# Performance work log

Measured on AMD Instinct MI355X. Metric: run time of the kernel, lower is better.

## Reference

```python
import jax, jax.numpy as jnp
import numpy as np

N = 100000
E = 1600000
F_IN = 128
DIM = 32
NUM_CLASSES = 40
BN_EPS = 1e-5


def setup_inputs() -> dict:
    key = jax.random.key(0)
    ks = jax.random.split(key, 16)
    inp = {}
    inp['x'] = jax.random.normal(ks[0], (N, F_IN), dtype=jnp.float32)
    inp['edge_index'] = jax.random.randint(ks[1], (2, E), 0, N, dtype=jnp.int64)
    s = lambda fan_in: 1.0 / np.sqrt(fan_in)
    # GINConv 1 MLP: Linear(F_IN, DIM) -> ReLU -> Linear(DIM, DIM)
    inp['w1a'] = jax.random.uniform(ks[2], (F_IN, DIM), jnp.float32, -s(F_IN), s(F_IN))
    inp['b1a'] = jnp.zeros((DIM,), jnp.float32)
    inp['w1b'] = jax.random.uniform(ks[3], (DIM, DIM), jnp.float32, -s(DIM), s(DIM))
    inp['b1b'] = jnp.zeros((DIM,), jnp.float32)
    # GINConv 2 MLP: Linear(DIM, DIM) -> ReLU -> Linear(DIM, DIM)
    inp['w2a'] = jax.random.uniform(ks[4], (DIM, DIM), jnp.float32, -s(DIM), s(DIM))
    inp['b2a'] = jnp.zeros((DIM,), jnp.float32)
    inp['w2b'] = jax.random.uniform(ks[5], (DIM, DIM), jnp.float32, -s(DIM), s(DIM))
    inp['b2b'] = jnp.zeros((DIM,), jnp.float32)
    # BatchNorm params (eval mode: running stats)
    inp['bn1_g'] = jnp.ones((DIM,), jnp.float32)
    inp['bn1_b'] = jnp.zeros((DIM,), jnp.float32)
    inp['bn1_m'] = jax.random.normal(ks[6], (DIM,), jnp.float32) * 0.1
    inp['bn1_v'] = jax.random.uniform(ks[7], (DIM,), jnp.float32, 0.5, 1.5)
    inp['bn2_g'] = jnp.ones((DIM,), jnp.float32)
    inp['bn2_b'] = jnp.zeros((DIM,), jnp.float32)
    inp['bn2_m'] = jax.random.normal(ks[8], (DIM,), jnp.float32) * 0.1
    inp['bn2_v'] = jax.random.uniform(ks[9], (DIM,), jnp.float32, 0.5, 1.5)
    # FC heads
    inp['fc1_w'] = jax.random.uniform(ks[10], (DIM, DIM), jnp.float32, -s(DIM), s(DIM))
    inp['fc1_b'] = jnp.zeros((DIM,), jnp.float32)
    inp['fc2_w'] = jax.random.uniform(ks[11], (DIM, NUM_CLASSES), jnp.float32, -s(DIM), s(DIM))
    inp['fc2_b'] = jnp.zeros((NUM_CLASSES,), jnp.float32)
    return inp


def _gin_conv(x, src, dst, wa, ba, wb, bb):
    # sum-aggregate neighbor features (messages flow src -> dst), eps = 0
    agg = jax.ops.segment_sum(x[src], dst, num_segments=N)
    h = agg + x  # (1 + eps) * x + sum_j x_j
    h = jax.nn.relu(h @ wa + ba)
    return h @ wb + bb


def _bn(x, g, b, m, v):
    return (x - m) * (g * jax.lax.rsqrt(v + BN_EPS)) + b


def reference(x, edge_index, w1a, b1a, w1b, b1b, w2a, b2a, w2b, b2b,
              bn1_g, bn1_b, bn1_m, bn1_v, bn2_g, bn2_b, bn2_m, bn2_v,
              fc1_w, fc1_b, fc2_w, fc2_b):
    src, dst = edge_index[0], edge_index[1]
    h = jax.nn.relu(_gin_conv(x, src, dst, w1a, b1a, w1b, b1b))
    h = _bn(h, bn1_g, bn1_b, bn1_m, bn1_v)  # dropout is identity in eval
    h = _gin_conv(h, src, dst, w2a, b2a, w2b, b2b)
    h = _bn(h, bn2_g, bn2_b, bn2_m, bn2_v)
    h = jax.nn.relu(h @ fc1_w + fc1_b)
    logits = h @ fc2_w + fc2_b
    return jax.nn.log_softmax(logits, axis=1)
```

## Files before the change

### kernel.cpp

```cpp
#include <hip/hip_runtime.h>
#include <hip/hip_bf16.h>

static constexpr int N_   = 100000;
static constexpr int E_   = 1600000;
static constexpr int FIN_ = 128;
static constexpr int DIM_ = 32;
static constexpr int NC_  = 40;
static constexpr int NB_BKT = (N_ + 127) / 128;
static constexpr int NCHUNK = 256;
static constexpr int EPC    = E_ / NCHUNK;
static constexpr int PROJ_NB = N_ / 32;
static constexpr int CS_NB  = (NB_BKT + 7) / 8;

__device__ __forceinline__ int edge_at(const void* e, int is64, long long i) {
    return is64 ? (int)((const long long*)e)[i] : ((const int*)e)[i];
}

__device__ __forceinline__ float bflo(unsigned u) { return __uint_as_float(u << 16); }
__device__ __forceinline__ float bfhi(unsigned u) { return __uint_as_float(u & 0xffff0000u); }

#define DETECT_FLAG(edge, sflag)                                        \
    if (threadIdx.x < 64) {                                             \
        const long long* p_ = (const long long*)(edge);                 \
        long long v_ = p_[threadIdx.x];                                 \
        bool bad_ = (v_ < 0 || v_ >= (long long)N_);                    \
        unsigned long long m_ = __ballot(bad_);                         \
        if (threadIdx.x == 0) sflag = (m_ == 0ull) ? 1 : 0;             \
    }                                                                   \
    __syncthreads();

__global__ __launch_bounds__(256) void chist_kernel(const void* __restrict__ edge,
                                                    int* __restrict__ ghist) {
    __shared__ int lh[NB_BKT];
    __shared__ int sflag;
    DETECT_FLAG(edge, sflag)
    for (int i = threadIdx.x; i < NB_BKT; i += 256) lh[i] = 0;
    __syncthreads();
    int f = sflag;
    int b = blockIdx.x;
    int end = b * EPC + EPC;
    for (int e = b * EPC + threadIdx.x; e < end; e += 256) {
        int d = edge_at(edge, f, (long long)E_ + e);
        atomicAdd(&lh[d >> 7], 1);
    }
    __syncthreads();
    for (int i = threadIdx.x; i < NB_BKT; i += 256) ghist[b * NB_BKT + i] = lh[i];
}

__global__ __launch_bounds__(256) void colscan_kernel(const int* __restrict__ ghist,
                                                      int* __restrict__ gcur,
                                                      int* __restrict__ bcnt,
                                                      int* __restrict__ bbase,
                                                      int* __restrict__ offs,
                                                      int* __restrict__ done) {
    __shared__ int tile[256 * 9];
    __shared__ int a[256];
    __shared__ int lastFlag;
    int tid = threadIdx.x;
    int k0 = blockIdx.x * 8;

    {
        int kk = tid & 7, r0 = tid >> 3;
        for (int p = 0; p < 8; ++p) {
            int b = r0 + p * 32;
            int k = k0 + kk;
            tile[b * 9 + kk] = (k < NB_BKT) ? ghist[b * NB_BKT + k] : 0;
        }
    }
    __syncthreads();

    int c = tid >> 5, lane = tid & 31;
    int v[8]; int s = 0;
#pragma unroll
    for (int r = 0; r < 8; ++r) { v[r] = tile[(lane * 8 + r) * 9 + c]; s += v[r]; }
    int incl = s;
#pragma unroll
    for (int off = 1; off < 32; off <<= 1) {
        int u = __shfl_up(incl, off, 32);
        if (lane >= off) incl += u;
    }
    int ex = incl - s;
    int k = k0 + c;
    if (k < NB_BKT) {
        int run = ex;
#pragma unroll
        for (int r = 0; r < 8; ++r) {
            int b = lane * 8 + r;
            gcur[b * NB_BKT + k] = run;
            run += v[r];
        }
        if (lane == 31) bcnt[k] = run;
    }
    __syncthreads();
    if (tid == 0) {
        __threadfence();
        int old = atomicAdd(done, 1);
        lastFlag = (old == CS_NB - 1) ? 1 : 0;
    }
    __syncthreads();
    if (lastFlag) {
        __threadfence();
        int b4[4]; int base4 = tid * 4; int t = 0;
#pragma unroll
        for (int j = 0; j < 4; ++j) { int i = base4 + j; b4[j] = (i < NB_BKT) ? bcnt[i] : 0; t += b4[j]; }
        a[tid] = t;
        __syncthreads();
        for (int off = 1; off < 256; off <<= 1) {
            int u = a[tid] + ((tid >= off) ? a[tid - off] : 0);
            __syncthreads(); a[tid] = u; __syncthreads();
        }
        int g = a[tid] - t;
#pragma unroll
        for (int j = 0; j < 4; ++j) { int i = base4 + j; if (i < NB_BKT) bbase[i] = g; g += b4[j]; }
        if (tid == 255) offs[N_] = a[255];
    }
}

__global__ __launch_bounds__(256) void dscatter_kernel(const void* __restrict__ edge,
                                                       const int* __restrict__ bbase,
                                                       const int* __restrict__ gcur,
                                                       int* __restrict__ packed) {
    __shared__ int cur[NB_BKT];
    __shared__ int sflag;
    DETECT_FLAG(edge, sflag)
    int b = blockIdx.x, tid = threadIdx.x;
    for (int k = tid; k < NB_BKT; k += 256) cur[k] = bbase[k] + gcur[b * NB_BKT + k];
    __syncthreads();
    int f = sflag;
    int end = b * EPC + EPC;
    for (int e = b * EPC + tid; e < end; e += 256) {
        int s = edge_at(edge, f, e);
        int d = edge_at(edge, f, (long long)E_ + e);
        int pos = atomicAdd(&cur[d >> 7], 1);
        packed[pos] = s | ((d & 127) << 17);
    }
}

__global__ __launch_bounds__(256) void fat_kernel(const int* __restrict__ bcnt,
                                                  const int* __restrict__ bbase,
                                                  const int* __restrict__ packed,
                                                  int* __restrict__ offs,
                                                  int* __restrict__ csr,
                                                  const float* __restrict__ x,
                                                  const float* __restrict__ w,
                                                  __hip_bfloat16* __restrict__ yh) {
    __shared__ __align__(16) char smem[32768];
    int tid = threadIdx.x;
    if (blockIdx.x < NB_BKT) {
        int* c   = (int*)smem;
        int* cur = (int*)smem + 128;
        int b = blockIdx.x;
        int beg = bbase[b], cnt = bcnt[b];
        if (tid < 128) c[tid] = 0;
        __syncthreads();
        for (int i = tid; i < cnt; i += 256)
            atomicAdd(&c[packed[beg + i] >> 17], 1);
        __syncthreads();
        int myv = (tid < 128) ? c[tid] : 0;
        for (int off = 1; off < 128; off <<= 1) {
            int t = 0;
            if (tid < 128) t = c[tid] + ((tid >= off) ? c[tid - off] : 0);
            __syncthreads();
            if (tid < 128) c[tid] = t;
            __syncthreads();
        }
        if (tid < 128) {
            int ex = c[tid] - myv;
            cur[tid] = ex;
            int node = b * 128 + tid;
            if (node < N_) offs[node] = beg + ex;
        }
        __syncthreads();
        for (int i = tid; i < cnt; i += 256) {
            int v = packed[beg + i];
            int p = atomicAdd(&cur[v >> 17], 1);
            csr[beg + p] = v & 0x1FFFF;
        }
    } else {
        float* wsm = (float*)smem;
        float* xs  = (float*)(smem + 16384);
        const float4* w4 = (const float4*)w;
        float4* ws4 = (float4*)wsm;
        for (int i = tid; i < FIN_ * DIM_ / 4; i += 256) ws4[i] = w4[i];

        int nodeBase = (blockIdx.x - NB_BKT) * 32;
        const float4* x4 = (const float4*)(x + (size_t)nodeBase * FIN_);
        float4* xs4 = (float4*)xs;
        for (int i = tid; i < 32 * FIN_ / 4; i += 256) xs4[i] = x4[i];
        __syncthreads();

        int d = tid & 31, ns = tid >> 5;
        for (int rep = 0; rep < 4; ++rep) {
            int node = ns + rep * 8;
            float acc = 0.f;
#pragma unroll 4
            for (int k = 0; k < FIN_; ++k) acc += xs[node * FIN_ + k] * wsm[k * DIM_ + d];
            yh[(size_t)(nodeBase + node) * DIM_ + d] = __float2bfloat16(acc);
        }
    }
}

__device__ __forceinline__ void gather_row(const int* __restrict__ csr,
                                           const char* __restrict__ vb,
                                           int beg, int end, int loff,
                                           float& a0, float& a1, float& a2, float& a3) {
    int i = beg;
    for (; i + 3 < end; i += 4) {
        int s0 = csr[i], s1 = csr[i + 1], s2 = csr[i + 2], s3 = csr[i + 3];
        uint2 u0 = *(const uint2*)(vb + (((size_t)s0) << 6) + loff);
        uint2 u1 = *(const uint2*)(vb + (((size_t)s1) << 6) + loff);
        uint2 u2 = *(const uint2*)(vb + (((size_t)s2) << 6) + loff);
        uint2 u3 = *(const uint2*)(vb + (((size_t)s3) << 6) + loff);
        a0 += (bflo(u0.x) + bflo(u1.x)) + (bflo(u2.x) + bflo(u3.x));
        a1 += (bfhi(u0.x) + bfhi(u1.x)) + (bfhi(u2.x) + bfhi(u3.x));
        a2 += (bflo(u0.y) + bflo(u1.y)) + (bflo(u2.y) + bflo(u3.y));
        a3 += (bfhi(u0.y) + bfhi(u1.y)) + (bfhi(u2.y) + bfhi(u3.y));
    }
    for (; i < end; ++i) {
        int s0 = csr[i];
        uint2 u0 = *(const uint2*)(vb + (((size_t)s0) << 6) + loff);
        a0 += bflo(u0.x); a1 += bfhi(u0.x); a2 += bflo(u0.y); a3 += bfhi(u0.y);
    }
}

__global__ __launch_bounds__(256) void aggmlp1_kernel(const int* __restrict__ offs,
                                                      const int* __restrict__ csr,
                                                      const __hip_bfloat16* __restrict__ yh,
                                                      const float* __restrict__ b1a,
                                                      const float* __restrict__ w1b,
                                                      const float* __restrict__ b1b,
                                                      const float* __restrict__ g1,
                                                      const float* __restrict__ be1,
                                                      const float* __restrict__ m1,
                                                      const float* __restrict__ v1,
                                                      const float* __restrict__ w2a,
                                                      __hip_bfloat16* __restrict__ zh) {
    __shared__ float A[32 * 33];
    __shared__ float B[32 * 33];
    __shared__ float w1s[DIM_ * DIM_];
    __shared__ float w2s[DIM_ * DIM_];
    int tid = threadIdx.x;
    for (int i = tid; i < DIM_ * DIM_; i += 256) { w1s[i] = w1b[i]; w2s[i] = w2a[i]; }

    int nl = tid >> 3, lane = tid & 7;
    int node = blockIdx.x * 32 + nl;
    int beg = offs[node], end = offs[node + 1];
    float a0 = 0.f, a1 = 0.f, a2 = 0.f, a3 = 0.f;
    gather_row(csr, (const char*)yh, beg, end, lane << 3, a0, a1, a2, a3);
    {
        float* p = &A[nl * 33 + lane * 4];
        p[0] = a0; p[1] = a1; p[2] = a2; p[3] = a3;
    }
    __syncthreads();

    int d = tid & 31, ng = tid >> 5;
    size_t gbase = (size_t)blockIdx.x * 32 * DIM_;

#pragma unroll
    for (int r = 0; r < 4; ++r) {
        int n = r * 8 + ng;
        float yv = __bfloat162float(yh[gbase + n * DIM_ + d]);
        A[n * 33 + d] = fmaxf(A[n * 33 + d] + yv + b1a[d], 0.f);
    }
    __syncthreads();

    float sc1 = g1[d] * rsqrtf(v1[d] + 1e-5f);
    float sh1 = be1[d] - m1[d] * sc1;

#pragma unroll
    for (int r = 0; r < 4; ++r) {
        int n = r * 8 + ng;
        float s = b1b[d];
#pragma unroll
        for (int k = 0; k < DIM_; ++k) s += A[n * 33 + k] * w1s[k * DIM_ + d];
        B[n * 33 + d] = fmaxf(s, 0.f) * sc1 + sh1;
    }
    __syncthreads();

#pragma unroll
    for (int r = 0; r < 4; ++r) {
        int n = r * 8 + ng;
        float s = 0.f;
#pragma unroll
        for (int k = 0; k < DIM_; ++k) s += B[n * 33 + k] * w2s[k * DIM_ + d];
        zh[gbase + n * DIM_ + d] = __float2bfloat16(s);
    }
}

__global__ __launch_bounds__(256) void aggmlp2_kernel(const int* __restrict__ offs,
                                                      const int* __restrict__ csr,
                                                      const __hip_bfloat16* __restrict__ zh,
                                                      const float* __restrict__ b2a,
                                                      const float* __restrict__ w2b,
                                                      const float* __restrict__ b2b,
                                                      const float* __restrict__ g2,
                                                      const float* __restrict__ be2,
                                                      const float* __restrict__ m2,
                                                      const float* __restrict__ v2,
                                                      const float* __restrict__ f1w,
                                                      const float* __restrict__ f1b,
                                                      const float* __restrict__ f2w,
                                                      const float* __restrict__ f2b,
                                                      float* __restrict__ out) {
    __shared__ float A[32 * 33];
    __shared__ float BC[DIM_ * NC_];
    __shared__ float wA[DIM_ * DIM_];
    __shared__ float wB[DIM_ * DIM_];
    int tid = threadIdx.x;
    for (int i = tid; i < DIM_ * DIM_; i += 256) { wA[i] = w2b[i]; wB[i] = f1w[i]; }

    int nl = tid >> 3, lane = tid & 7;
    int node = blockIdx.x * 32 + nl;
    int beg = offs[node], end = offs[node + 1];
    float a0 = 0.f, a1 = 0.f, a2 = 0.f, a3 = 0.f;
    gather_row(csr, (const char*)zh, beg, end, lane << 3, a0, a1, a2, a3);
    {
        float* p = &A[nl * 33 + lane * 4];
        p[0] = a0; p[1] = a1; p[2] = a2; p[3] = a3;
    }
    __syncthreads();

    int d = tid & 31, ng = tid >> 5;
    size_t gbase = (size_t)blockIdx.x * 32 * DIM_;

#pragma unroll
    for (int r = 0; r < 4; ++r) {
        int n = r * 8 + ng;
        float zv = __bfloat162float(zh[gbase + n * DIM_ + d]);
        A[n * 33 + d] = fmaxf(A[n * 33 + d] + zv + b2a[d], 0.f);
    }
    __syncthreads();

    float sc2 = g2[d] * rsqrtf(v2[d] + 1e-5f);
    float sh2 = be2[d] - m2[d] * sc2;

#pragma unroll
    for (int r = 0; r < 4; ++r) {
        int n = r * 8 + ng;
        float s = b2b[d];
#pragma unroll
        for (int k = 0; k < DIM_; ++k) s += A[n * 33 + k] * wA[k * DIM_ + d];
        BC[n * 33 + d] = s * sc2 + sh2;
    }
    __syncthreads();

#pragma unroll
    for (int r = 0; r < 4; ++r) {
        int n = r * 8 + ng;
        float s = f1b[d];
#pragma unroll
        for (int k = 0; k < DIM_; ++k) s += BC[n * 33 + k] * wB[k * DIM_ + d];
        A[n * 33 + d] = fmaxf(s, 0.f);
    }
    __syncthreads();
    for (int i = tid; i < DIM_ * NC_; i += 256) BC[i] = f2w[i];
    __syncthreads();

    int c2 = 32 + (d & 7);
#pragma unroll
    for (int r = 0; r < 4; ++r) {
        int n = r * 8 + ng;
        float l0 = f2b[d];
        float l1 = f2b[c2];
#pragma unroll
        for (int k = 0; k < DIM_; ++k) {
            float fv = A[n * 33 + k];
            l0 += fv * BC[k * NC_ + d];
            l1 += fv * BC[k * NC_ + c2];
        }
        float mx = fmaxf(l0, l1);
#pragma unroll
        for (int off = 16; off; off >>= 1) mx = fmaxf(mx, __shfl_xor(mx, off));
        float se = __expf(l0 - mx) + ((d < 8) ? __expf(l1 - mx) : 0.f);
#pragma unroll
        for (int off = 16; off; off >>= 1) se += __shfl_xor(se, off);
        float lse = mx + __logf(se);
        size_t ob = (size_t)(blockIdx.x * 32 + n) * NC_;
        out[ob + d] = l0 - lse;
        if (d < 8) out[ob + 32 + d] = l1 - lse;
    }
}

extern "C" void kernel_launch(void* const* d_in, const int* in_sizes, int n_in,
                              void* d_out, int out_size, void* d_ws, size_t ws_size,
                              hipStream_t stream) {
    const float* x   = (const float*)d_in[0];
    const void*  edg = d_in[1];
    const float* w1a = (const float*)d_in[2];
    const float* b1a = (const float*)d_in[3];
    const float* w1b = (const float*)d_in[4];
    const float* b1b = (const float*)d_in[5];
    const float* w2a = (const float*)d_in[6];
    const float* b2a = (const float*)d_in[7];
    const float* w2b = (const float*)d_in[8];
    const float* b2b = (const float*)d_in[9];
    const float* g1  = (const float*)d_in[10];
    const float* be1 = (const float*)d_in[11];
    const float* m1  = (const float*)d_in[12];
    const float* v1  = (const float*)d_in[13];
    const float* g2  = (const float*)d_in[14];
    const float* be2 = (const float*)d_in[15];
    const float* m2  = (const float*)d_in[16];
    const float* v2  = (const float*)d_in[17];
    const float* f1w = (const float*)d_in[18];
    const float* f1b = (const float*)d_in[19];
    const float* f2w = (const float*)d_in[20];
    const float* f2b = (const float*)d_in[21];
    float* out = (float*)d_out;

    char* ws = (char*)d_ws;
    int* done   = (int*)ws;
    int* bcnt   = (int*)(ws + 256);
    int* bbase  = (int*)(ws + 3584);
    int* ghist  = (int*)(ws + 6912);
    int* gcur   = (int*)(ws + 807680);
    int* offs   = (int*)(ws + 1608448);
    int* packed = (int*)(ws + 2008576);
    int* csr    = (int*)(ws + 8408576);
    __hip_bfloat16* yh = (__hip_bfloat16*)(ws + 14808576);
    __hip_bfloat16* zh = (__hip_bfloat16*)(ws + 21208576);

    hipMemsetAsync(done, 0, 4, stream);

    chist_kernel<<<NCHUNK, 256, 0, stream>>>(edg, ghist);
    colscan_kernel<<<CS_NB, 256, 0, stream>>>(ghist, gcur, bcnt, bbase, offs, done);
    dscatter_kernel<<<NCHUNK, 256, 0, stream>>>(edg, bbase, gcur, packed);
    fat_kernel<<<NB_BKT + PROJ_NB, 256, 0, stream>>>(bcnt, bbase, packed, offs, csr,
                                                     x, w1a, yh);

    aggmlp1_kernel<<<N_ / 32, 256, 0, stream>>>(offs, csr, yh, b1a, w1b, b1b,
                                                g1, be1, m1, v1, w2a, zh);

    aggmlp2_kernel<<<N_ / 32, 256, 0, stream>>>(offs, csr, zh, b2a, w2b, b2b,
                                                g2, be2, m2, v2, f1w, f1b,
                                                f2w, f2b, out);
}
```

Baseline: 325.7 us.

## Drop full CSR build; aggregate per 32-node bucket with shared-memory atomics

Shrinks destination buckets from 128 to 32 nodes so each bucket matches one MLP block of 32 nodes. The per-bucket CSR sort kernel is removed, and the aggregation kernels read the bucket-packed edges directly, accumulating neighbor features into shared memory with float atomics. The x@W1a projection is merged into the histogram kernel launch, and the MLP inner loops are register-blocked over four nodes with float4 shared reads. This removes one kernel and a full pass over the edges, but adds LDS atomic contention and makes the summation order nondeterministic.

```diff
diff --git a/kernel.cpp b/kernel.cpp
--- a/kernel.cpp
+++ b/kernel.cpp
@@ -6,7 +6,8 @@
 static constexpr int FIN_ = 128;
 static constexpr int DIM_ = 32;
 static constexpr int NC_  = 40;
-static constexpr int NB_BKT = (N_ + 127) / 128;
+static constexpr int BKT    = 32;
+static constexpr int NB_BKT = N_ / BKT;
 static constexpr int NCHUNK = 256;
 static constexpr int EPC    = E_ / NCHUNK;
 static constexpr int PROJ_NB = N_ / 32;
@@ -29,29 +30,71 @@
     }                                                                   \
     __syncthreads();
 
-__global__ __launch_bounds__(256) void chist_kernel(const void* __restrict__ edge,
-                                                    int* __restrict__ ghist) {
-    __shared__ int lh[NB_BKT];
+__global__ __launch_bounds__(256) void histproj_kernel(const void* __restrict__ edge,
+                                                       int* __restrict__ ghist,
+                                                       const float* __restrict__ x,
+                                                       const float* __restrict__ w,
+                                                       __hip_bfloat16* __restrict__ yh) {
+    __shared__ __align__(16) char smem[32768];
     __shared__ int sflag;
-    DETECT_FLAG(edge, sflag)
-    for (int i = threadIdx.x; i < NB_BKT; i += 256) lh[i] = 0;
-    __syncthreads();
-    int f = sflag;
-    int b = blockIdx.x;
-    int end = b * EPC + EPC;
-    for (int e = b * EPC + threadIdx.x; e < end; e += 256) {
-        int d = edge_at(edge, f, (long long)E_ + e);
-        atomicAdd(&lh[d >> 7], 1);
-    }
-    __syncthreads();
-    for (int i = threadIdx.x; i < NB_BKT; i += 256) ghist[b * NB_BKT + i] = lh[i];
+    int tid = threadIdx.x;
+    if (blockIdx.x < NCHUNK) {
+        int* lh = (int*)smem;
+        DETECT_FLAG(edge, sflag)
+        for (int i = tid; i < NB_BKT; i += 256) lh[i] = 0;
+        __syncthreads();
+        int f = sflag;
+        int b = blockIdx.x;
+        int end = b * EPC + EPC;
+        for (int e = b * EPC + tid; e < end; e += 256) {
+            int d = edge_at(edge, f, (long long)E_ + e);
+            atomicAdd(&lh[d >> 5], 1);
+        }
+        __syncthreads();
+        for (int i = tid; i < NB_BKT; i += 256) ghist[b * NB_BKT + i] = lh[i];
+    } else {
+        float* wsm = (float*)smem;
+        float* xs  = (float*)(smem + 16384);
+        const float4* w4 = (const float4*)w;
+        float4* ws4 = (float4*)wsm;
+        for (int i = tid; i < FIN_ * DIM_ / 4; i += 256) ws4[i] = w4[i];
+
+        int nodeBase = (blockIdx.x - NCHUNK) * 32;
+        const float4* x4 = (const float4*)(x + (size_t)nodeBase * FIN_);
+        float4* xs4 = (float4*)xs;
+        for (int i = tid; i < 32 * FIN_ / 4; i += 256) xs4[i] = x4[i];
+        __syncthreads();
+
+        int d = tid & 31, ns = tid >> 5;
+        float acc0 = 0.f, acc1 = 0.f, acc2 = 0.f, acc3 = 0.f;
+        const float4* r0 = (const float4*)&xs[(ns +  0) * FIN_];
+        const float4* r1 = (const float4*)&xs[(ns +  8) * FIN_];
+        const float4* r2 = (const float4*)&xs[(ns + 16) * FIN_];
+        const float4* r3 = (const float4*)&xs[(ns + 24) * FIN_];
+#pragma unroll
+        for (int kc = 0; kc < FIN_ / 4; ++kc) {
+            float w0 = wsm[(kc * 4 + 0) * DIM_ + d];
+            float w1 = wsm[(kc * 4 + 1) * DIM_ + d];
+            float w2 = wsm[(kc * 4 + 2) * DIM_ + d];
+            float w3 = wsm[(kc * 4 + 3) * DIM_ + d];
+            float4 a;
+            a = r0[kc]; acc0 += a.x * w0 + a.y * w1 + a.z * w2 + a.w * w3;
+            a = r1[kc]; acc1 += a.x * w0 + a.y * w1 + a.z * w2 + a.w * w3;
+            a = r2[kc]; acc2 += a.x * w0 + a.y * w1 + a.z * w2 + a.w * w3;
+            a = r3[kc]; acc3 += a.x * w0 + a.y * w1 + a.z * w2 + a.w * w3;
+        }
+        __hip_bfloat16* yo = yh + (size_t)nodeBase * DIM_ + d;
+        yo[(ns +  0) * DIM_] = __float2bfloat16(acc0);
+        yo[(ns +  8) * DIM_] = __float2bfloat16(acc1);
+        yo[(ns + 16) * DIM_] = __float2bfloat16(acc2);
+        yo[(ns + 24) * DIM_] = __float2bfloat16(acc3);
+    }
 }
 
 __global__ __launch_bounds__(256) void colscan_kernel(const int* __restrict__ ghist,
                                                       int* __restrict__ gcur,
                                                       int* __restrict__ bcnt,
                                                       int* __restrict__ bbase,
-                                                      int* __restrict__ offs,
                                                       int* __restrict__ done) {
     __shared__ int tile[256 * 9];
     __shared__ int a[256];
@@ -100,9 +143,10 @@
     __syncthreads();
     if (lastFlag) {
         __threadfence();
-        int b4[4]; int base4 = tid * 4; int t = 0;
-#pragma unroll
-        for (int j = 0; j < 4; ++j) { int i = base4 + j; b4[j] = (i < NB_BKT) ? bcnt[i] : 0; t += b4[j]; }
+        constexpr int IPT = (NB_BKT + 255) / 256;
+        int bj[IPT]; int base = tid * IPT; int t = 0;
+#pragma unroll
+        for (int j = 0; j < IPT; ++j) { int i = base + j; bj[j] = (i < NB_BKT) ? bcnt[i] : 0; t += bj[j]; }
         a[tid] = t;
         __syncthreads();
         for (int off = 1; off < 256; off <<= 1) {
@@ -111,8 +155,7 @@
         }
         int g = a[tid] - t;
 #pragma unroll
-        for (int j = 0; j < 4; ++j) { int i = base4 + j; if (i < NB_BKT) bbase[i] = g; g += b4[j]; }
-        if (tid == 255) offs[N_] = a[255];
+        for (int j = 0; j < IPT; ++j) { int i = base + j; if (i < NB_BKT) bbase[i] = g; g += bj[j]; }
     }
 }
 
@@ -131,243 +174,272 @@
     for (int e = b * EPC + tid; e < end; e += 256) {
         int s = edge_at(edge, f, e);
         int d = edge_at(edge, f, (long long)E_ + e);
-        int pos = atomicAdd(&cur[d >> 7], 1);
-        packed[pos] = s | ((d & 127) << 17);
-    }
-}
-
-__global__ __launch_bounds__(256) void fat_kernel(const int* __restrict__ bcnt,
-                                                  const int* __restrict__ bbase,
-                                                  const int* __restrict__ packed,
-                                                  int* __restrict__ offs,
-                                                  int* __restrict__ csr,
-                                                  const float* __restrict__ x,
-                                                  const float* __restrict__ w,
-                                                  __hip_bfloat16* __restrict__ yh) {
-    __shared__ __align__(16) char smem[32768];
-    int tid = threadIdx.x;
-    if (blockIdx.x < NB_BKT) {
-        int* c   = (int*)smem;
-        int* cur = (int*)smem + 128;
-        int b = blockIdx.x;
-        int beg = bbase[b], cnt = bcnt[b];
-        if (tid < 128) c[tid] = 0;
-        __syncthreads();
-        for (int i = tid; i < cnt; i += 256)
-            atomicAdd(&c[packed[beg + i] >> 17], 1);
-        __syncthreads();
-        int myv = (tid < 128) ? c[tid] : 0;
-        for (int off = 1; off < 128; off <<= 1) {
-            int t = 0;
-            if (tid < 128) t = c[tid] + ((tid >= off) ? c[tid - off] : 0);
-            __syncthreads();
-            if (tid < 128) c[tid] = t;
-            __syncthreads();
-        }
-        if (tid < 128) {
-            int ex = c[tid] - myv;
-            cur[tid] = ex;
-            int node = b * 128 + tid;
-            if (node < N_) offs[node] = beg + ex;
-        }
-        __syncthreads();
-        for (int i = tid; i < cnt; i += 256) {
-            int v = packed[beg + i];
-            int p = atomicAdd(&cur[v >> 17], 1);
-            csr[beg + p] = v & 0x1FFFF;
-        }
-    } else {
-        float* wsm = (float*)smem;
-        float* xs  = (float*)(smem + 16384);
-        const float4* w4 = (const float4*)w;
-        float4* ws4 = (float4*)wsm;
-        for (int i = tid; i < FIN_ * DIM_ / 4; i += 256) ws4[i] = w4[i];
-
-        int nodeBase = (blockIdx.x - NB_BKT) * 32;
-        const float4* x4 = (const float4*)(x + (size_t)nodeBase * FIN_);
-        float4* xs4 = (float4*)xs;
-        for (int i = tid; i < 32 * FIN_ / 4; i += 256) xs4[i] = x4[i];
-        __syncthreads();
-
-        int d = tid & 31, ns = tid >> 5;
-        for (int rep = 0; rep < 4; ++rep) {
-            int node = ns + rep * 8;
-            float acc = 0.f;
-#pragma unroll 4
-            for (int k = 0; k < FIN_; ++k) acc += xs[node * FIN_ + k] * wsm[k * DIM_ + d];
-            yh[(size_t)(nodeBase + node) * DIM_ + d] = __float2bfloat16(acc);
-        }
-    }
-}
-
-__device__ __forceinline__ void gather_row(const int* __restrict__ csr,
-                                           const char* __restrict__ vb,
-                                           int beg, int end, int loff,
-                                           float& a0, float& a1, float& a2, float& a3) {
-    int i = beg;
-    for (; i + 3 < end; i += 4) {
-        int s0 = csr[i], s1 = csr[i + 1], s2 = csr[i + 2], s3 = csr[i + 3];
-        uint2 u0 = *(const uint2*)(vb + (((size_t)s0) << 6) + loff);
-        uint2 u1 = *(const uint2*)(vb + (((size_t)s1) << 6) + loff);
-        uint2 u2 = *(const uint2*)(vb + (((size_t)s2) << 6) + loff);
-        uint2 u3 = *(const uint2*)(vb + (((size_t)s3) << 6) + loff);
-        a0 += (bflo(u0.x) + bflo(u1.x)) + (bflo(u2.x) + bflo(u3.x));
-        a1 += (bfhi(u0.x) + bfhi(u1.x)) + (bfhi(u2.x) + bfhi(u3.x));
-        a2 += (bflo(u0.y) + bflo(u1.y)) + (bflo(u2.y) + bflo(u3.y));
-        a3 += (bfhi(u0.y) + bfhi(u1.y)) + (bfhi(u2.y) + bfhi(u3.y));
-    }
-    for (; i < end; ++i) {
-        int s0 = csr[i];
-        uint2 u0 = *(const uint2*)(vb + (((size_t)s0) << 6) + loff);
-        a0 += bflo(u0.x); a1 += bfhi(u0.x); a2 += bflo(u0.y); a3 += bfhi(u0.y);
-    }
-}
-
-__global__ __launch_bounds__(256) void aggmlp1_kernel(const int* __restrict__ offs,
-                                                      const int* __restrict__ csr,
-                                                      const __hip_bfloat16* __restrict__ yh,
-                                                      const float* __restrict__ b1a,
-                                                      const float* __restrict__ w1b,
-                                                      const float* __restrict__ b1b,
-                                                      const float* __restrict__ g1,
-                                                      const float* __restrict__ be1,
-                                                      const float* __restrict__ m1,
-                                                      const float* __restrict__ v1,
-                                                      const float* __restrict__ w2a,
-                                                      __hip_bfloat16* __restrict__ zh) {
-    __shared__ float A[32 * 33];
-    __shared__ float B[32 * 33];
+        int pos = atomicAdd(&cur[d >> 5], 1);
+        packed[pos] = s | ((d & 31) << 17);
+    }
+}
+
+__device__ __forceinline__ void edge_gather(const int* __restrict__ packed,
+                                            const char* __restrict__ vb,
+                                            float* __restrict__ A,
+                                            int beg, int end, int tid) {
+    int slot = tid & 7;
+    int loff = slot << 3;
+    int co   = slot << 2;
+    int i = beg + (tid >> 3);
+    for (; i + 32 < end; i += 64) {
+        int p0 = packed[i];
+        int p1 = packed[i + 32];
+        uint2 u0 = *(const uint2*)(vb + (((size_t)(p0 & 0x1FFFF)) << 6) + loff);
+        uint2 u1 = *(const uint2*)(vb + (((size_t)(p1 & 0x1FFFF)) << 6) + loff);
+        float* dp0 = &A[(p0 >> 17) * 36 + co];
+        atomicAdd(dp0 + 0, bflo(u0.x)); atomicAdd(dp0 + 1, bfhi(u0.x));
+        atomicAdd(dp0 + 2, bflo(u0.y)); atomicAdd(dp0 + 3, bfhi(u0.y));
+        float* dp1 = &A[(p1 >> 17) * 36 + co];
+        atomicAdd(dp1 + 0, bflo(u1.x)); atomicAdd(dp1 + 1, bfhi(u1.x));
+        atomicAdd(dp1 + 2, bflo(u1.y)); atomicAdd(dp1 + 3, bfhi(u1.y));
+    }
+    if (i < end) {
+        int p0 = packed[i];
+        uint2 u0 = *(const uint2*)(vb + (((size_t)(p0 & 0x1FFFF)) << 6) + loff);
+        float* dp0 = &A[(p0 >> 17) * 36 + co];
+        atomicAdd(dp0 + 0, bflo(u0.x)); atomicAdd(dp0 + 1, bfhi(u0.x));
+        atomicAdd(dp0 + 2, bflo(u0.y)); atomicAdd(dp0 + 3, bfhi(u0.y));
+    }
+}
+
+__global__ __launch_bounds__(256, 8) void aggmlp1_kernel(const int* __restrict__ bbase,
+                                                         const int* __restrict__ bcnt,
+                                                         const int* __restrict__ packed,
+                                                         const __hip_bfloat16* __restrict__ yh,
+                                                         const float* __restrict__ b1a,
+                                                         const float* __restrict__ w1b,
+                                                         const float* __restrict__ b1b,
+                                                         const float* __restrict__ g1,
+                                                         const float* __restrict__ be1,
+                                                         const float* __restrict__ m1,
+                                                         const float* __restrict__ v1,
+                                                         const float* __restrict__ w2a,
+                                                         __hip_bfloat16* __restrict__ zh) {
+    __shared__ float A[32 * 36];
+    __shared__ float B[32 * 36];
     __shared__ float w1s[DIM_ * DIM_];
     __shared__ float w2s[DIM_ * DIM_];
     int tid = threadIdx.x;
+    for (int i = tid; i < 32 * 36; i += 256) A[i] = 0.f;
     for (int i = tid; i < DIM_ * DIM_; i += 256) { w1s[i] = w1b[i]; w2s[i] = w2a[i]; }
-
-    int nl = tid >> 3, lane = tid & 7;
-    int node = blockIdx.x * 32 + nl;
-    int beg = offs[node], end = offs[node + 1];
-    float a0 = 0.f, a1 = 0.f, a2 = 0.f, a3 = 0.f;
-    gather_row(csr, (const char*)yh, beg, end, lane << 3, a0, a1, a2, a3);
-    {
-        float* p = &A[nl * 33 + lane * 4];
-        p[0] = a0; p[1] = a1; p[2] = a2; p[3] = a3;
-    }
+    __syncthreads();
+
+    int b = blockIdx.x;
+    int beg = bbase[b], end = beg + bcnt[b];
+    edge_gather(packed, (const char*)yh, A, beg, end, tid);
     __syncthreads();
 
     int d = tid & 31, ng = tid >> 5;
-    size_t gbase = (size_t)blockIdx.x * 32 * DIM_;
-
-#pragma unroll
-    for (int r = 0; r < 4; ++r) {
-        int n = r * 8 + ng;
-        float yv = __bfloat162float(yh[gbase + n * DIM_ + d]);
-        A[n * 33 + d] = fmaxf(A[n * 33 + d] + yv + b1a[d], 0.f);
+    size_t gbase = (size_t)b * 32 * DIM_;
+
+    {
+        float bv = b1a[d];
+#pragma unroll
+        for (int r = 0; r < 4; ++r) {
+            int n = r * 8 + ng;
+            float yv = __bfloat162float(yh[gbase + n * DIM_ + d]);
+            A[n * 36 + d] = fmaxf(A[n * 36 + d] + yv + bv, 0.f);
+        }
     }
     __syncthreads();
 
     float sc1 = g1[d] * rsqrtf(v1[d] + 1e-5f);
     float sh1 = be1[d] - m1[d] * sc1;
 
-#pragma unroll
-    for (int r = 0; r < 4; ++r) {
-        int n = r * 8 + ng;
-        float s = b1b[d];
-#pragma unroll
-        for (int k = 0; k < DIM_; ++k) s += A[n * 33 + k] * w1s[k * DIM_ + d];
-        B[n * 33 + d] = fmaxf(s, 0.f) * sc1 + sh1;
-    }
-    __syncthreads();
-
-#pragma unroll
-    for (int r = 0; r < 4; ++r) {
-        int n = r * 8 + ng;
-        float s = 0.f;
-#pragma unroll
-        for (int k = 0; k < DIM_; ++k) s += B[n * 33 + k] * w2s[k * DIM_ + d];
-        zh[gbase + n * DIM_ + d] = __float2bfloat16(s);
-    }
-}
-
-__global__ __launch_bounds__(256) void aggmlp2_kernel(const int* __restrict__ offs,
-                                                      const int* __restrict__ csr,
-                                                      const __hip_bfloat16* __restrict__ zh,
-                                                      const float* __restrict__ b2a,
-                                                      const float* __restrict__ w2b,
-                                                      const float* __restrict__ b2b,
-                                                      const float* __restrict__ g2,
-                                                      const float* __restrict__ be2,
-                                                      const float* __restrict__ m2,
-                                                      const float* __restrict__ v2,
-                                                      const float* __restrict__ f1w,
-                                                      const float* __restrict__ f1b,
-                                                      const float* __restrict__ f2w,
-                                                      const float* __restrict__ f2b,
-                                                      float* __restrict__ out) {
-    __shared__ float A[32 * 33];
+    {
+        float s0 = b1b[d], s1 = s0, s2 = s0, s3 = s0;
+        const float4* r0 = (const float4*)&A[(ng +  0) * 36];
+        const float4* r1 = (const float4*)&A[(ng +  8) * 36];
+        const float4* r2 = (const float4*)&A[(ng + 16) * 36];
+        const float4* r3 = (const float4*)&A[(ng + 24) * 36];
+#pragma unroll
+        for (int kc = 0; kc < 8; ++kc) {
+            float w0 = w1s[(kc * 4 + 0) * DIM_ + d];
+            float w1 = w1s[(kc * 4 + 1) * DIM_ + d];
+            float w2 = w1s[(kc * 4 + 2) * DIM_ + d];
+            float w3 = w1s[(kc * 4 + 3) * DIM_ + d];
+            float4 a;
+            a = r0[kc]; s0 += a.x * w0 + a.y * w1 + a.z * w2 + a.w * w3;
+            a = r1[kc]; s1 += a.x * w0 + a.y * w1 + a.z * w2 + a.w * w3;
+            a = r2[kc]; s2 += a.x * w0 + a.y * w1 + a.z * w2 + a.w * w3;
+            a = r3[kc]; s3 += a.x * w0 + a.y * w1 + a.z * w2 + a.w * w3;
+        }
+        B[(ng +  0) * 36 + d] = fmaxf(s0, 0.f) * sc1 + sh1;
+        B[(ng +  8) * 36 + d] = fmaxf(s1, 0.f) * sc1 + sh1;
+        B[(ng + 16) * 36 + d] = fmaxf(s2, 0.f) * sc1 + sh1;
+        B[(ng + 24) * 36 + d] = fmaxf(s3, 0.f) * sc1 + sh1;
+    }
+    __syncthreads();
+
+    {
+        float s0 = 0.f, s1 = 0.f, s2 = 0.f, s3 = 0.f;
+        const float4* r0 = (const float4*)&B[(ng +  0) * 36];
+        const float4* r1 = (const float4*)&B[(ng +  8) * 36];
+        const float4* r2 = (const float4*)&B[(ng + 16) * 36];
+        const float4* r3 = (const float4*)&B[(ng + 24) * 36];
+#pragma unroll
+        for (int kc = 0; kc < 8; ++kc) {
+            float w0 = w2s[(kc * 4 + 0) * DIM_ + d];
+            float w1 = w2s[(kc * 4 + 1) * DIM_ + d];
+            float w2 = w2s[(kc * 4 + 2) * DIM_ + d];
+            float w3 = w2s[(kc * 4 + 3) * DIM_ + d];
+            float4 a;
+            a = r0[kc]; s0 += a.x * w0 + a.y * w1 + a.z * w2 + a.w * w3;
+            a = r1[kc]; s1 += a.x * w0 + a.y * w1 + a.z * w2 + a.w * w3;
+            a = r2[kc]; s2 += a.x * w0 + a.y * w1 + a.z * w2 + a.w * w3;
+            a = r3[kc]; s3 += a.x * w0 + a.y * w1 + a.z * w2 + a.w * w3;
+        }
+        zh[gbase + (ng +  0) * DIM_ + d] = __float2bfloat16(s0);
+        zh[gbase + (ng +  8) * DIM_ + d] = __float2bfloat16(s1);
+        zh[gbase + (ng + 16) * DIM_ + d] = __float2bfloat16(s2);
+        zh[gbase + (ng + 24) * DIM_ + d] = __float2bfloat16(s3);
+    }
+}
+
+__global__ __launch_bounds__(256, 8) void aggmlp2_kernel(const int* __restrict__ bbase,
+                                                         const int* __restrict__ bcnt,
+                                                         const int* __restrict__ packed,
+                                                         const __hip_bfloat16* __restrict__ zh,
+                                                         const float* __restrict__ b2a,
+                                                         const float* __restrict__ w2b,
+                                                         const float* __restrict__ b2b,
+                                                         const float* __restrict__ g2,
+                                                         const float* __restrict__ be2,
+                                                         const float* __restrict__ m2,
+                                                         const float* __restrict__ v2,
+                                                         const float* __restrict__ f1w,
+                                                         const float* __restrict__ f1b,
+                                                         const float* __restrict__ f2w,
+                                                         const float* __restrict__ f2b,
+                                                         float* __restrict__ out) {
+    __shared__ float A[32 * 36];
     __shared__ float BC[DIM_ * NC_];
     __shared__ float wA[DIM_ * DIM_];
     __shared__ float wB[DIM_ * DIM_];
     int tid = threadIdx.x;
+    for (int i = tid; i < 32 * 36; i += 256) A[i] = 0.f;
     for (int i = tid; i < DIM_ * DIM_; i += 256) { wA[i] = w2b[i]; wB[i] = f1w[i]; }
-
-    int nl = tid >> 3, lane = tid & 7;
-    int node = blockIdx.x * 32 + nl;
-    int beg = offs[node], end = offs[node + 1];
-    float a0 = 0.f, a1 = 0.f, a2 = 0.f, a3 = 0.f;
-    gather_row(csr, (const char*)zh, beg, end, lane << 3, a0, a1, a2, a3);
-    {
-        float* p = &A[nl * 33 + lane * 4];
-        p[0] = a0; p[1] = a1; p[2] = a2; p[3] = a3;
-    }
+    __syncthreads();
+
+    int b = blockIdx.x;
+    int beg = bbase[b], end = beg + bcnt[b];
+    edge_gather(packed, (const char*)zh, A, beg, end, tid);
     __syncthreads();
 
     int d = tid & 31, ng = tid >> 5;
-    size_t gbase = (size_t)blockIdx.x * 32 * DIM_;
-
-#pragma unroll
-    for (int r = 0; r < 4; ++r) {
-        int n = r * 8 + ng;
-        float zv = __bfloat162float(zh[gbase + n * DIM_ + d]);
-        A[n * 33 + d] = fmaxf(A[n * 33 + d] + zv + b2a[d], 0.f);
+    size_t gbase = (size_t)b * 32 * DIM_;
+
+    {
+        float bv = b2a[d];
+#pragma unroll
+        for (int r = 0; r < 4; ++r) {
+            int n = r * 8 + ng;
+            float zv = __bfloat162float(zh[gbase + n * DIM_ + d]);
+            A[n * 36 + d] = fmaxf(A[n * 36 + d] + zv + bv, 0.f);
+        }
     }
     __syncthreads();
 
     float sc2 = g2[d] * rsqrtf(v2[d] + 1e-5f);
     float sh2 = be2[d] - m2[d] * sc2;
 
+    {
+        float s0 = b2b[d], s1 = s0, s2 = s0, s3 = s0;
+        const float4* r0 = (const float4*)&A[(ng +  0) * 36];
+        const float4* r1 = (const float4*)&A[(ng +  8) * 36];
+        const float4* r2 = (const float4*)&A[(ng + 16) * 36];
+        const float4* r3 = (const float4*)&A[(ng + 24) * 36];
+#pragma unroll
+        for (int kc = 0; kc < 8; ++kc) {
+            float w0 = wA[(kc * 4 + 0) * DIM_ + d];
+            float w1 = wA[(kc * 4 + 1) * DIM_ + d];
+            float w2 = wA[(kc * 4 + 2) * DIM_ + d];
+            float w3 = wA[(kc * 4 + 3) * DIM_ + d];
+            float4 a;
+            a = r0[kc]; s0 += a.x * w0 + a.y * w1 + a.z * w2 + a.w * w3;
+            a = r1[kc]; s1 += a.x * w0 + a.y * w1 + a.z * w2 + a.w * w3;
+            a = r2[kc]; s2 += a.x * w0 + a.y * w1 + a.z * w2 + a.w * w3;
+            a = r3[kc]; s3 += a.x * w0 + a.y * w1 + a.z * w2 + a.w * w3;
+        }
+        BC[(ng +  0) * 36 + d] = s0 * sc2 + sh2;
+        BC[(ng +  8) * 36 + d] = s1 * sc2 + sh2;
+        BC[(ng + 16) * 36 + d] = s2 * sc2 + sh2;
+        BC[(ng + 24) * 36 + d] = s3 * sc2 + sh2;
+    }
+    __syncthreads();
+
+    {
+        float s0 = f1b[d], s1 = s0, s2 = s0, s3 = s0;
+        const float4* r0 = (const float4*)&BC[(ng +  0) * 36];
+        const float4* r1 = (const float4*)&BC[(ng +  8) * 36];
+        const float4* r2 = (const float4*)&BC[(ng + 16) * 36];
+        const float4* r3 = (const float4*)&BC[(ng + 24) * 36];
+#pragma unroll
+        for (int kc = 0; kc < 8; ++kc) {
+            float w0 = wB[(kc * 4 + 0) * DIM_ + d];
+            float w1 = wB[(kc * 4 + 1) * DIM_ + d];
+            float w2 = wB[(kc * 4 + 2) * DIM_ + d];
+            float w3 = wB[(kc * 4 + 3) * DIM_ + d];
+            float4 a;
+            a = r0[kc]; s0 += a.x * w0 + a.y * w1 + a.z * w2 + a.w * w3;
+            a = r1[kc]; s1 += a.x * w0 + a.y * w1 + a.z * w2 + a.w * w3;
+            a = r2[kc]; s2 += a.x * w0 + a.y * w1 + a.z * w2 + a.w * w3;
+            a = r3[kc]; s3 += a.x * w0 + a.y * w1 + a.z * w2 + a.w * w3;
+        }
+        A[(ng +  0) * 36 + d] = fmaxf(s0, 0.f);
+        A[(ng +  8) * 36 + d] = fmaxf(s1, 0.f);
+        A[(ng + 16) * 36 + d] = fmaxf(s2, 0.f);
+        A[(ng + 24) * 36 + d] = fmaxf(s3, 0.f);
+    }
+    __syncthreads();
+    for (int i = tid; i < DIM_ * NC_; i += 256) BC[i] = f2w[i];
+    __syncthreads();
+
+    int c2 = 32 + (d & 7);
+    float l00 = f2b[d], l01 = l00, l02 = l00, l03 = l00;
+    float cb = f2b[c2];
+    float l10 = cb, l11 = cb, l12 = cb, l13 = cb;
+    {
+        const float4* r0 = (const float4*)&A[(ng +  0) * 36];
+        const float4* r1 = (const float4*)&A[(ng +  8) * 36];
+        const float4* r2 = (const float4*)&A[(ng + 16) * 36];
+        const float4* r3 = (const float4*)&A[(ng + 24) * 36];
+#pragma unroll
+        for (int kc = 0; kc < 8; ++kc) {
+            float wa0 = BC[(kc * 4 + 0) * NC_ + d];
+            float wa1 = BC[(kc * 4 + 1) * NC_ + d];
+            float wa2 = BC[(kc * 4 + 2) * NC_ + d];
+            float wa3 = BC[(kc * 4 + 3) * NC_ + d];
+            float wb0 = BC[(kc * 4 + 0) * NC_ + c2];
+            float wb1 = BC[(kc * 4 + 1) * NC_ + c2];
+            float wb2 = BC[(kc * 4 + 2) * NC_ + c2];
+            float wb3 = BC[(kc * 4 + 3) * NC_ + c2];
+            float4 a;
+            a = r0[kc];
+            l00 += a.x * wa0 + a.y * wa1 + a.z * wa2 + a.w * wa3;
+            l10 += a.x * wb0 + a.y * wb1 + a.z * wb2 + a.w * wb3;
+            a = r1[kc];
+            l01 += a.x * wa0 + a.y * wa1 + a.z * wa2 + a.w * wa3;
+            l11 += a.x * wb0 + a.y * wb1 + a.z * wb2 + a.w * wb3;
+            a = r2[kc];
+            l02 += a.x * wa0 + a.y * wa1 + a.z * wa2 + a.w * wa3;
+            l12 += a.x * wb0 + a.y * wb1 + a.z * wb2 + a.w * wb3;
+            a = r3[kc];
+            l03 += a.x * wa0 + a.y * wa1 + a.z * wa2 + a.w * wa3;
+            l13 += a.x * wb0 + a.y * wb1 + a.z * wb2 + a.w * wb3;
+        }
+    }
 #pragma unroll
     for (int r = 0; r < 4; ++r) {
+        float l0 = (r == 0) ? l00 : (r == 1) ? l01 : (r == 2) ? l02 : l03;
+        float l1 = (r == 0) ? l10 : (r == 1) ? l11 : (r == 2) ? l12 : l13;
         int n = r * 8 + ng;
-        float s = b2b[d];
-#pragma unroll
-        for (int k = 0; k < DIM_; ++k) s += A[n * 33 + k] * wA[k * DIM_ + d];
-        BC[n * 33 + d] = s * sc2 + sh2;
-    }
-    __syncthreads();
-
-#pragma unroll
-    for (int r = 0; r < 4; ++r) {
-        int n = r * 8 + ng;
-        float s = f1b[d];
-#pragma unroll
-        for (int k = 0; k < DIM_; ++k) s += BC[n * 33 + k] * wB[k * DIM_ + d];
-        A[n * 33 + d] = fmaxf(s, 0.f);
-    }
-    __syncthreads();
-    for (int i = tid; i < DIM_ * NC_; i += 256) BC[i] = f2w[i];
-    __syncthreads();
-
-    int c2 = 32 + (d & 7);
-#pragma unroll
-    for (int r = 0; r < 4; ++r) {
-        int n = r * 8 + ng;
-        float l0 = f2b[d];
-        float l1 = f2b[c2];
-#pragma unroll
-        for (int k = 0; k < DIM_; ++k) {
-            float fv = A[n * 33 + k];
-            l0 += fv * BC[k * NC_ + d];
-            l1 += fv * BC[k * NC_ + c2];
-        }
         float mx = fmaxf(l0, l1);
 #pragma unroll
         for (int off = 16; off; off >>= 1) mx = fmaxf(mx, __shfl_xor(mx, off));
@@ -375,7 +447,7 @@
 #pragma unroll
         for (int off = 16; off; off >>= 1) se += __shfl_xor(se, off);
         float lse = mx + __logf(se);
-        size_t ob = (size_t)(blockIdx.x * 32 + n) * NC_;
+        size_t ob = (size_t)(b * 32 + n) * NC_;
         out[ob + d] = l0 - lse;
         if (d < 8) out[ob + 32 + d] = l1 - lse;
     }
@@ -411,27 +483,23 @@
     char* ws = (char*)d_ws;
     int* done   = (int*)ws;
     int* bcnt   = (int*)(ws + 256);
-    int* bbase  = (int*)(ws + 3584);
-    int* ghist  = (int*)(ws + 6912);
-    int* gcur   = (int*)(ws + 807680);
-    int* offs   = (int*)(ws + 1608448);
-    int* packed = (int*)(ws + 2008576);
-    int* csr    = (int*)(ws + 8408576);
-    __hip_bfloat16* yh = (__hip_bfloat16*)(ws + 14808576);
-    __hip_bfloat16* zh = (__hip_bfloat16*)(ws + 21208576);
+    int* bbase  = (int*)(ws + 12800);
+    int* ghist  = (int*)(ws + 25344);
+    int* gcur   = (int*)(ws + 3225344);
+    int* packed = (int*)(ws + 6425344);
+    __hip_bfloat16* yh = (__hip_bfloat16*)(ws + 12825344);
+    __hip_bfloat16* zh = (__hip_bfloat16*)(ws + 19225344);
 
     hipMemsetAsync(done, 0, 4, stream);
 
-    chist_kernel<<<NCHUNK, 256, 0, stream>>>(edg, ghist);
-    colscan_kernel<<<CS_NB, 256, 0, stream>>>(ghist, gcur, bcnt, bbase, offs, done);
+    histproj_kernel<<<NCHUNK + PROJ_NB, 256, 0, stream>>>(edg, ghist, x, w1a, yh);
+    colscan_kernel<<<CS_NB, 256, 0, stream>>>(ghist, gcur, bcnt, bbase, done);
     dscatter_kernel<<<NCHUNK, 256, 0, stream>>>(edg, bbase, gcur, packed);
-    fat_kernel<<<NB_BKT + PROJ_NB, 256, 0, stream>>>(bcnt, bbase, packed, offs, csr,
-                                                     x, w1a, yh);
-
-    aggmlp1_kernel<<<N_ / 32, 256, 0, stream>>>(offs, csr, yh, b1a, w1b, b1b,
-                                                g1, be1, m1, v1, w2a, zh);
-
-    aggmlp2_kernel<<<N_ / 32, 256, 0, stream>>>(offs, csr, zh, b2a, w2b, b2b,
-                                                g2, be2, m2, v2, f1w, f1b,
-                                                f2w, f2b, out);
-}
+
+    aggmlp1_kernel<<<NB_BKT, 256, 0, stream>>>(bbase, bcnt, packed, yh, b1a, w1b, b1b,
+                                               g1, be1, m1, v1, w2a, zh);
+
+    aggmlp2_kernel<<<NB_BKT, 256, 0, stream>>>(bbase, bcnt, packed, zh, b2a, w2b, b2b,
+                                               g2, be2, m2, v2, f1w, f1b,
+                                               f2w, f2b, out);
+}
```

New measurement: 839.4 us. +157.7%, slower.
